# Optimization experiments

Measured on AMD Instinct MI355X. Metric: run time of the kernel, lower is better.

## Reference

```python
import jax, jax.numpy as jnp
import numpy as np

B, T = 32, 64
STOCH, DETER, HIDDEN = 1024, 4096, 1024
ACT_DIM, EMBED = 128, 1536
MIN_STD = 0.1
EPS = 1e-3  # dreamerv3-torch uses LayerNorm(eps=1e-3)


def _ln(x, g, b):
    m = jnp.mean(x, -1, keepdims=True)
    v = jnp.var(x, -1, keepdims=True)
    return (x - m) * jax.lax.rsqrt(v + EPS) * g + b


def setup_inputs() -> dict:
    key = jax.random.key(0)
    ks = jax.random.split(key, 24)

    def w(k, fan_in, fan_out):
        return jax.random.normal(k, (fan_in, fan_out), jnp.float32) / np.sqrt(fan_in)

    inp = {
        "embed": jax.random.normal(ks[0], (B, T, EMBED), jnp.float32),
        "action": jax.random.normal(ks[1], (B, T, ACT_DIM), jnp.float32),
        "is_first": jnp.zeros((B, T), jnp.bool_),
        "init_deter": jax.random.normal(ks[2], (B, DETER), jnp.float32),
        "init_stoch": jax.random.normal(ks[3], (B, STOCH), jnp.float32),
        "noise_prior": jax.random.normal(ks[4], (B, T, STOCH), jnp.float32),
        "noise_post": jax.random.normal(ks[5], (B, T, STOCH), jnp.float32),
        # _img_in_layers: Linear(stoch+act -> hidden, no bias) + LN + SiLU
        "W_in": w(ks[6], STOCH + ACT_DIM, HIDDEN),
        "g_in": 1.0 + 0.1 * jax.random.normal(ks[7], (HIDDEN,), jnp.float32),
        "b_in": 0.1 * jax.random.normal(ks[8], (HIDDEN,), jnp.float32),
        # GRUCell: Linear(hidden+deter -> 3*deter, no bias) + LN
        "W_gru": w(ks[9], HIDDEN + DETER, 3 * DETER),
        "g_gru": 1.0 + 0.1 * jax.random.normal(ks[10], (3 * DETER,), jnp.float32),
        "b_gru": 0.1 * jax.random.normal(ks[11], (3 * DETER,), jnp.float32),
        # _img_out_layers: Linear(deter -> hidden, no bias) + LN + SiLU
        "W_imgout": w(ks[12], DETER, HIDDEN),
        "g_io": 1.0 + 0.1 * jax.random.normal(ks[13], (HIDDEN,), jnp.float32),
        "b_io": 0.1 * jax.random.normal(ks[14], (HIDDEN,), jnp.float32),
        # _obs_out_layers: Linear(deter+embed -> hidden, no bias) + LN + SiLU
        "W_obsout": w(ks[15], DETER + EMBED, HIDDEN),
        "g_oo": 1.0 + 0.1 * jax.random.normal(ks[16], (HIDDEN,), jnp.float32),
        "b_oo": 0.1 * jax.random.normal(ks[17], (HIDDEN,), jnp.float32),
        # suff-stats layers: Linear(hidden -> 2*stoch) with bias
        "W_ims": w(ks[18], HIDDEN, 2 * STOCH),
        "b_ims": 0.01 * jax.random.normal(ks[19], (2 * STOCH,), jnp.float32),
        "W_obs": w(ks[20], HIDDEN, 2 * STOCH),
        "b_obs": 0.01 * jax.random.normal(ks[21], (2 * STOCH,), jnp.float32),
    }
    return inp


def _observe(embed, action, init_deter, init_stoch, noise_prior, noise_post,
             W_in, g_in, b_in, W_gru, g_gru, b_gru, W_imgout, g_io, b_io,
             W_obsout, g_oo, b_oo, W_ims, b_ims, W_obs, b_obs):
    def suff_stats(h, W, b, noise):
        stats = h @ W + b
        mean, std = jnp.split(stats, 2, -1)
        std = jax.nn.softplus(std) + MIN_STD  # std_act='softplus', mean_act='none'
        return mean, std, mean + std * noise

    def step(carry, xs):
        deter, stoch = carry
        e, a, n_p, n_q = xs
        # img_in: concat(prev_stoch, action) -> Linear -> LN -> SiLU
        x = jax.nn.silu(_ln(jnp.concatenate([stoch, a], -1) @ W_in, g_in, b_in))
        # GRUCell with layernorm (update_bias = -1)
        parts = _ln(jnp.concatenate([x, deter], -1) @ W_gru, g_gru, b_gru)
        reset, cand, update = jnp.split(parts, 3, -1)
        reset = jax.nn.sigmoid(reset)
        cand = jnp.tanh(reset * cand)
        update = jax.nn.sigmoid(update - 1.0)
        deter = update * cand + (1.0 - update) * deter
        # prior (imagination) suff stats + sample
        h_p = jax.nn.silu(_ln(deter @ W_imgout, g_io, b_io))
        mean_p, std_p, stoch_p = suff_stats(h_p, W_ims, b_ims, n_p)
        # posterior (observation) suff stats + sample
        h_q = jax.nn.silu(_ln(jnp.concatenate([deter, e], -1) @ W_obsout, g_oo, b_oo))
        mean_q, std_q, stoch_q = suff_stats(h_q, W_obs, b_obs, n_q)
        out = jnp.concatenate([deter, stoch_q, mean_q, std_q, stoch_p, mean_p, std_p], -1)
        return (deter, stoch_q), out

    xs = (jnp.swapaxes(embed, 0, 1), jnp.swapaxes(action, 0, 1),
          jnp.swapaxes(noise_prior, 0, 1), jnp.swapaxes(noise_post, 0, 1))
    _, outs = jax.lax.scan(step, (init_deter, init_stoch), xs)
    return jnp.swapaxes(outs, 0, 1)  # [B, T, deter + 6*stoch]


def reference(embed, action, is_first, init_deter, init_stoch, noise_prior, noise_post,
              W_in, g_in, b_in, W_gru, g_gru, b_gru, W_imgout, g_io, b_io,
              W_obsout, g_oo, b_oo, W_ims, b_ims, W_obs, b_obs):
    # is_first is all-False and state is given, so the init-mixing branch is never taken
    del is_first
    return _observe(embed, action, init_deter, init_stoch, noise_prior, noise_post,
                    W_in, g_in, b_in, W_gru, g_gru, b_gru, W_imgout, g_io, b_io,
                    W_obsout, g_oo, b_oo, W_ims, b_ims, W_obs, b_obs)
```

## Files before the change

### kernel.cpp

```cpp
#include <hip/hip_runtime.h>
#include <hip/hip_bf16.h>

#define T_ 64
#define DETER_ 4096
#define GRUN 12288

typedef __attribute__((ext_vector_type(8))) __bf16 bf16x8;
typedef __attribute__((ext_vector_type(4))) float f32x4;
typedef __attribute__((ext_vector_type(8))) unsigned short u16x8;
typedef __attribute__((ext_vector_type(4))) unsigned short u16x4;

__device__ inline unsigned short f2bf(float f) {
    union { float f; unsigned u; } x; x.f = f;
    unsigned r = x.u + 0x7fffu + ((x.u >> 16) & 1u);
    return (unsigned short)(r >> 16);
}
__device__ inline float sigmoidf_(float v) { return 1.f / (1.f + __expf(-v)); }
__device__ inline float siluf_(float v)    { return v / (1.f + __expf(-v)); }
__device__ inline float softplusf_(float v){ return fmaxf(v, 0.f) + __logf(1.f + __expf(-fabsf(v))); }
__device__ inline float tanhf_(float v)    { return 2.f / (1.f + __expf(-2.f * v)) - 1.f; }

__device__ inline void barrier_() {
    asm volatile("" ::: "memory");
    __builtin_amdgcn_s_barrier();
    asm volatile("" ::: "memory");
}
template <int N> __device__ inline void vmwaitN() {
    asm volatile("s_waitcnt vmcnt(%0)" :: "i"(N) : "memory");
}
__device__ inline void lgkmwait_() {
    asm volatile("s_waitcnt lgkmcnt(0)" ::: "memory");
}


__global__ __launch_bounds__(256) void k_pack(const float* __restrict__ W,
                                              unsigned short* __restrict__ dst,
                                              int K, int N) {
    long fid = (long)blockIdx.x * 256 + threadIdx.x;
    long nfr = (long)K * N / 8;
    if (fid >= nfr) return;
    int lane = (int)(fid & 63);
    long tile = fid >> 6;
    int ktiles = K >> 5;
    int k_t = (int)(tile % ktiles);
    int n_t = (int)(tile / ktiles);
    int c = lane & 15, kb = lane >> 4;
    int k0 = k_t * 32 + kb * 8;
    int n = n_t * 16 + c;
    unsigned short v[8];
#pragma unroll
    for (int i = 0; i < 8; i++) v[i] = f2bf(W[(long)(k0 + i) * N + n]);
    *reinterpret_cast<u16x8*>(dst + fid * 8) = *reinterpret_cast<u16x8*>(v);
}

__global__ __launch_bounds__(256) void k_conv(const float* __restrict__ s,
                                              unsigned short* __restrict__ d, long n) {
    long i = ((long)blockIdx.x * 256 + threadIdx.x) * 4;
    if (i >= n) return;
    f32x4 v = *reinterpret_cast<const f32x4*>(s + i);
    unsigned short o[4];
#pragma unroll
    for (int k = 0; k < 4; k++) o[k] = f2bf(v[k]);
    *reinterpret_cast<u16x4*>(d + i) = *reinterpret_cast<u16x4*>(o);
}

__global__ __launch_bounds__(256) void k_copy(const float* __restrict__ s,
                                              float* __restrict__ d, long n) {
    long i = ((long)blockIdx.x * 256 + threadIdx.x) * 4;
    if (i >= n) return;
    *reinterpret_cast<f32x4*>(d + i) = *reinterpret_cast<const f32x4*>(s + i);
}


template <int CW>
__device__ inline void stage_glds(unsigned short* chunk, const unsigned short* __restrict__ src,
                                  long ld, long k0) {
    constexpr int NI = (32 * CW * 2) / 4096;
    int wv = (int)threadIdx.x >> 6, lane = (int)threadIdx.x & 63;
#pragma unroll
    for (int i = 0; i < NI; ++i) {
        int obase = (wv * NI + i) << 10;
        int o = obase + lane * 16;
        int row = o / (CW * 2);
        int cb = o - row * (CW * 2);
        int gb = cb ^ ((row & 7) << 4);
        const char* ga = (const char*)(src + (long)row * ld + k0) + gb;
        __builtin_amdgcn_global_load_lds(
            (const __attribute__((address_space(1))) void*)ga,
            (__attribute__((address_space(3))) void*)(chunk + (obase >> 1)),
            16, 0, 0);
    }
}

__device__ inline void stage_ln512(unsigned short* chunk, const float* __restrict__ raw,
                                   int ld, int col0,
                                   const float* __restrict__ g, const float* __restrict__ b,
                                   const float* s_mean, const float* s_rstd) {
    int tid = threadIdx.x;
#pragma unroll
    for (int i = 0; i < 8; ++i) {
        int e = tid * 8 + i * 2048;
        int row = e >> 9, col = e & 511;
        float m = s_mean[row], rs = s_rstd[row];
// ... 121 lines not shown
                                       g_ln, b_ln, s_mean, s_rstd);
        if (ch < NG) { if (nx < NG) vmwaitN<NI>(); else vmwaitN<0>(); }
        if (nx >= NG && nx < NCH) lgkmwait_();
        barrier_();
        int kt0 = (ch < NG) ? (ktg0 + ch * (CW / 32)) : ((ch - NG) * 16);
        mfma_rh<CW>(sb[ch & 1], mrow, kb, bbase + (long)kt0 * 512, acc);
        barrier_();
    }
    __syncthreads();
#pragma unroll
    for (int j = 0; j < 4; ++j) s_out[rh * 16 + kb * 4 + j][nt * 16 + c] = acc[j];
    __syncthreads();
    int orow = tid >> 3, c4 = (tid & 7) * 4;
    long rg = rowbase + orow;
    float v[4]; float s = 0.f, q = 0.f;
#pragma unroll
    for (int i = 0; i < 4; ++i) {
        float x = s_out[orow][c4 + i];
        if (addin) x += addin[rg * addin_ld + blockIdx.x * 32 + c4 + i];
        v[i] = x; s += x; q += x * x;
    }
#pragma unroll
    for (int i = 0; i < 4; ++i) outp[rg * out_ld + blockIdx.x * 32 + c4 + i] = v[i];
    if (partials) {
#pragma unroll
        for (int m = 1; m < 8; m <<= 1) { s += __shfl_xor(s, m); q += __shfl_xor(q, m); }
        if ((tid & 7) == 0) {
            partials[((long)blockIdx.x * prows + rg) * 2] = s;
            partials[((long)blockIdx.x * prows + rg) * 2 + 1] = q;
        }
    }
}

__global__ __launch_bounds__(256) void k_gru2(
    const unsigned short* __restrict__ Bp,
    const unsigned short* __restrict__ deterb,
    const float* __restrict__ x_raw, const float* __restrict__ px,
    const float* __restrict__ g_in, const float* __restrict__ b_in,
    float* __restrict__ Gp0, float* __restrict__ Gp1)
{
    __shared__ __align__(16) unsigned short sb[2][32 * 512];
    __shared__ float s_out[32][66];
    __shared__ float s_mean[32], s_rstd[32];
    int tid = threadIdx.x, lane = tid & 63, wv = tid >> 6;
    int c = lane & 15, kb = lane >> 4;
    long ntg = (long)blockIdx.x * 4 + wv;
    const unsigned short* bbase = Bp + ntg * 160 * 512 + lane * 8;
    f32x4 acc0 = {0,0,0,0}, acc1 = {0,0,0,0};

    if (blockIdx.y == 0) {
        if (tid < 32) {
            float s = 0.f, q = 0.f;
            for (int j = 0; j < 32; ++j) {
                s += px[((long)j * 32 + tid) * 2];
                q += px[((long)j * 32 + tid) * 2 + 1];
            }
            float m = s * (1.f / 1024.f);
            s_mean[tid] = m;
            s_rstd[tid] = rsqrtf(q * (1.f / 1024.f) - m * m + 1e-3f);
        }
        __syncthreads();
        stage_glds<512>(sb[0], deterb, 4096, 0);
        stage_glds<512>(sb[1], deterb, 4096, 512);
        vmwaitN<8>(); barrier_();
        mfma2<512>(sb[0], c, kb, bbase + 32 * 512, acc0, acc1);
        barrier_();
        stage_glds<512>(sb[0], deterb, 4096, 1024);
        vmwaitN<8>(); barrier_();
        mfma2<512>(sb[1], c, kb, bbase + 48 * 512, acc0, acc1);
        barrier_();
        stage_ln512(sb[1], x_raw, 1024, 0, g_in, b_in, s_mean, s_rstd);
        vmwaitN<0>(); barrier_();
        mfma2<512>(sb[0], c, kb, bbase + 64 * 512, acc0, acc1);
        barrier_();
        stage_ln512(sb[0], x_raw, 1024, 512, g_in, b_in, s_mean, s_rstd);
        lgkmwait_(); barrier_();
        mfma2<512>(sb[1], c, kb, bbase + 0, acc0, acc1);
        barrier_();
        mfma2<512>(sb[0], c, kb, bbase + 16 * 512, acc0, acc1);
    } else {
        stage_glds<512>(sb[0], deterb, 4096, 1536);
        stage_glds<512>(sb[1], deterb, 4096, 2048);
        vmwaitN<8>(); barrier_();
        mfma2<512>(sb[0], c, kb, bbase + 80 * 512, acc0, acc1);
        barrier_();
        stage_glds<512>(sb[0], deterb, 4096, 2560);
        vmwaitN<8>(); barrier_();
        mfma2<512>(sb[1], c, kb, bbase + 96 * 512, acc0, acc1);
        barrier_();
        stage_glds<512>(sb[1], deterb, 4096, 3072);
        vmwaitN<8>(); barrier_();
        mfma2<512>(sb[0], c, kb, bbase + 112 * 512, acc0, acc1);
        barrier_();
        stage_glds<512>(sb[0], deterb, 4096, 3584);
        vmwaitN<8>(); barrier_();
        mfma2<512>(sb[1], c, kb, bbase + 128 * 512, acc0, acc1);
        barrier_();
        vmwaitN<0>(); barrier_();
        mfma2<512>(sb[0], c, kb, bbase + 144 * 512, acc0, acc1);
    }
    __syncthreads();
#pragma unroll
    for (int j = 0; j < 4; ++j) {
        s_out[kb * 4 + j][wv * 16 + c] = acc0[j];
        s_out[16 + kb * 4 + j][wv * 16 + c] = acc1[j];
    }
    __syncthreads();
    float* G = (blockIdx.y == 0) ? Gp0 : Gp1;
    int row = tid >> 3, c8 = (tid & 7) * 8;
#pragma unroll
    for (int i = 0; i < 8; ++i)
        G[(long)row * GRUN + blockIdx.x * 64 + c8 + i] = s_out[row][c8 + i];
}

__global__ __launch_bounds__(1024) void k_deter2(
    const float* __restrict__ Gp0, const float* __restrict__ Gp1,
    const float* __restrict__ g_gru, const float* __restrict__ b_gru,
    float* __restrict__ deterf, unsigned short* __restrict__ deterb,
    unsigned short* __restrict__ deter_allb, float* __restrict__ out, int t)
{
    __shared__ float gsh[GRUN];
    __shared__ float red[32];
    int r = blockIdx.x, tid = threadIdx.x;
    int lane = tid & 63, wv = tid >> 6;
    const float* a0 = Gp0 + (long)r * GRUN;
    const float* a1 = Gp1 + (long)r * GRUN;
    float s = 0.f, q = 0.f;
#pragma unroll
    for (int i = 0; i < 3; ++i) {
        int col = (tid + i * 1024) * 4;
        f32x4 v = *reinterpret_cast<const f32x4*>(a0 + col);
        v += *reinterpret_cast<const f32x4*>(a1 + col);
        *reinterpret_cast<f32x4*>(gsh + col) = v;
#pragma unroll
        for (int j = 0; j < 4; ++j) { s += v[j]; q += v[j] * v[j]; }
    }
#pragma unroll
    for (int m = 1; m < 64; m <<= 1) { s += __shfl_xor(s, m); q += __shfl_xor(q, m); }
    if (lane == 0) { red[wv] = s; red[16 + wv] = q; }
    __syncthreads();
    float fs = 0.f, fq = 0.f;
#pragma unroll
    for (int i = 0; i < 16; ++i) { fs += red[i]; fq += red[16 + i]; }
    float mean = fs * (1.f / 12288.f);
    float rstd = rsqrtf(fq * (1.f / 12288.f) - mean * mean + 1e-3f);
    long orow = (long)r * T_ + t;
#pragma unroll
    for (int it = 0; it < 2; ++it) {
        int j = tid * 2 + it * 2048;
        float2 rr = *reinterpret_cast<const float2*>(gsh + j);
        float2 cc = *reinterpret_cast<const float2*>(gsh + 4096 + j);
        float2 uu = *reinterpret_cast<const float2*>(gsh + 8192 + j);
        float2 dd = *reinterpret_cast<const float2*>(deterf + (long)r * DETER_ + j);
        float dn[2]; unsigned short db[2];
#pragma unroll
        for (int i = 0; i < 2; ++i) {
            float gv = (i == 0) ? rr.x : rr.y;
            float cv = (i == 0) ? cc.x : cc.y;
            float uv = (i == 0) ? uu.x : uu.y;
            float dv = (i == 0) ? dd.x : dd.y;
            float lr = (gv - mean) * rstd * g_gru[j + i] + b_gru[j + i];
            float lc = (cv - mean) * rstd * g_gru[4096 + j + i] + b_gru[4096 + j + i];
            float lu = (uv - mean) * rstd * g_gru[8192 + j + i] + b_gru[8192 + j + i];
            float reset = sigmoidf_(lr);
            float cand = tanhf_(reset * lc);
            float upd = sigmoidf_(lu - 1.f);
            dn[i] = upd * cand + (1.f - upd) * dv;
            db[i] = f2bf(dn[i]);
        }
        float2 nd; nd.x = dn[0]; nd.y = dn[1];
        *reinterpret_cast<float2*>(deterf + (long)r * DETER_ + j) = nd;
        unsigned pk = (unsigned)db[0] | ((unsigned)db[1] << 16);
        *reinterpret_cast<unsigned*>(deterb + (long)r * DETER_ + j) = pk;
        *reinterpret_cast<unsigned*>(deter_allb + orow * DETER_ + j) = pk;
        *reinterpret_cast<float2*>(out + orow * 10240 + j) = nd;
    }
}

__global__ __launch_bounds__(256) void k_h4(
    const unsigned short* __restrict__ Wood,
    const unsigned short* __restrict__ deterb,
    float* __restrict__ hpart)
{
    __shared__ __align__(16) unsigned short sb[2][32 * 512];
    __shared__ float s_out[32][66];
    int tid = threadIdx.x, lane = tid & 63, wv = tid >> 6;
    int c = lane & 15, kb = lane >> 4;
    int n = blockIdx.x, kq = blockIdx.y;
    const unsigned short* bbase = Wood + ((long)(n * 4 + wv) * 128) * 512 + lane * 8;
    f32x4 acc0 = {0,0,0,0}, acc1 = {0,0,0,0};
    stage_glds<512>(sb[0], deterb, 4096, (long)kq * 1024);
    stage_glds<512>(sb[1], deterb, 4096, (long)kq * 1024 + 512);
    vmwaitN<8>(); barrier_();
    mfma2<512>(sb[0], c, kb, bbase + (long)(kq * 32) * 512, acc0, acc1);
    vmwaitN<0>(); barrier_();
    mfma2<512>(sb[1], c, kb, bbase + (long)(kq * 32 + 16) * 512, acc0, acc1);
    __syncthreads();
#pragma unroll
    for (int j = 0; j < 4; ++j) {
        s_out[kb * 4 + j][wv * 16 + c] = acc0[j];
        s_out[16 + kb * 4 + j][wv * 16 + c] = acc1[j];
    }
    __syncthreads();
    int row = tid >> 3, c8 = (tid & 7) * 8;
    float* hp = hpart + (long)kq * 32768 + (long)row * 1024 + n * 64 + c8;
#pragma unroll
    for (int i = 0; i < 8; ++i) hp[i] = s_out[row][c8 + i];
}

__global__ __launch_bounds__(256) void k_statsq2(
    const unsigned short* __restrict__ Bp, const float* __restrict__ hpart,
    const float* __restrict__ E_pre,
    const float* __restrict__ g_oo, const float* __restrict__ b_oo,
    const float* __restrict__ bias,
    const float* __restrict__ noise, float* __restrict__ out,
    unsigned short* __restrict__ stochb, int t)
{
    __shared__ __align__(16) unsigned short sb[2][32 * 512];
    __shared__ float s_out[32][66];
    __shared__ float s_mean[32], s_rstd[32];
    int tid = threadIdx.x, lane = tid & 63, wv = tid >> 6;
    int c = lane & 15, kb = lane >> 4;
    {
        int row = tid >> 3, c0 = (tid & 7) * 128;
        const float* h0 = hpart + (long)row * 1024 + c0;
        const float* ep = E_pre + ((long)row * T_ + t) * 1024 + c0;
        float s = 0.f, q = 0.f;
#pragma unroll 8
        for (int kk = 0; kk < 128; kk += 4) {
            f32x4 v = *reinterpret_cast<const f32x4*>(h0 + kk);
            v += *reinterpret_cast<const f32x4*>(h0 + 32768 + kk);
            v += *reinterpret_cast<const f32x4*>(h0 + 65536 + kk);
            v += *reinterpret_cast<const f32x4*>(h0 + 98304 + kk);
            v += *reinterpret_cast<const f32x4*>(ep + kk);
#pragma unroll
            for (int j2 = 0; j2 < 4; ++j2) { s += v[j2]; q += v[j2] * v[j2]; }
        }
#pragma unroll
        for (int m = 1; m < 8; m <<= 1) { s += __shfl_xor(s, m); q += __shfl_xor(q, m); }
        if ((tid & 7) == 0) {
            float mm = s * (1.f / 1024.f);
            s_mean[row] = mm;
            s_rstd[row] = rsqrtf(q * (1.f / 1024.f) - mm * mm + 1e-3f);
        }
    }
    __syncthreads();
    int part = wv >> 1, nt = wv & 1;
    long ntg = (long)part * 64 + blockIdx.x * 2 + nt;
    const unsigned short* bbase = Bp + ntg * 32 * 512 + lane * 8;
    f32x4 acc0 = {0,0,0,0}, acc1 = {0,0,0,0};
    stage_lnsum(sb[0], hpart, E_pre, t, 0, g_oo, b_oo, s_mean, s_rstd);
    stage_lnsum(sb[1], hpart, E_pre, t, 512, g_oo, b_oo, s_mean, s_rstd);
    lgkmwait_(); barrier_();
    mfma2<512>(sb[0], c, kb, bbase, acc0, acc1);
    mfma2<512>(sb[1], c, kb, bbase + 16 * 512, acc0, acc1);
    __syncthreads();
    float bv = bias[ntg * 16 + c];
#pragma unroll
    for (int j = 0; j < 4; ++j) {
        s_out[kb * 4 + j][part * 32 + nt * 16 + c] = acc0[j] + bv;
        s_out[16 + kb * 4 + j][part * 32 + nt * 16 + c] = acc1[j] + bv;
    }
    __syncthreads();
    int r = tid >> 3, j0 = (tid & 7) * 4;
    long orow = (long)r * T_ + t;
#pragma unroll
    for (int i = 0; i < 4; ++i) {
        int j = j0 + i;
        float mean = s_out[r][j];
        float sd = softplusf_(s_out[r][32 + j]) + 0.1f;
        int cg2 = blockIdx.x * 32 + j;
        float st = mean + sd * noise[orow * 1024 + cg2];
        float* op = out + orow * 10240;
        op[4096 + cg2] = st; op[5120 + cg2] = mean; op[6144 + cg2] = sd;
        stochb[(long)r * 1024 + cg2] = f2bf(st);
    }
}

__global__ __launch_bounds__(256) void k_bstats(
    const unsigned short* __restrict__ Bp, const unsigned short* __restrict__ h_pb,
    const float* __restrict__ bias, const float* __restrict__ noise,
    float* __restrict__ out)
{
    __shared__ __align__(16) unsigned short sb[2][32 * 512];
    __shared__ float s_out[32][66];
    int tid = threadIdx.x;
    int lane = tid & 63, wv = tid >> 6;
    int part = wv >> 1, nt = wv & 1;
    int c = lane & 15, kb = lane >> 4;
    int s_ = blockIdx.x, rowbase = blockIdx.y * 32;
    const unsigned short* A = h_pb + (long)rowbase * 1024;
    long ntg = (long)part * 64 + s_ * 2 + nt;
    const unsigned short* bbase = Bp + ntg * 32 * 512 + lane * 8;
    f32x4 acc0 = {0.f,0.f,0.f,0.f}, acc1 = {0.f,0.f,0.f,0.f};
    stage_glds<512>(sb[0], A, 1024, 0);
    stage_glds<512>(sb[1], A, 1024, 512);
    vmwaitN<8>(); barrier_();
    mfma_rh<512>(sb[0], c, kb, bbase, acc0);
    mfma_rh<512>(sb[0], 16 + c, kb, bbase, acc1);
    vmwaitN<0>(); barrier_();
    mfma_rh<512>(sb[1], c, kb, bbase + 16 * 512, acc0);
    mfma_rh<512>(sb[1], 16 + c, kb, bbase + 16 * 512, acc1);
    __syncthreads();
    float bv = bias[ntg * 16 + c];
#pragma unroll
    for (int j = 0; j < 4; ++j) {
        s_out[kb * 4 + j][part * 32 + nt * 16 + c] = acc0[j] + bv;
        s_out[16 + kb * 4 + j][part * 32 + nt * 16 + c] = acc1[j] + bv;
// ... 69 lines not shown
    float* out = (float*)d_out;

    char* ws = (char*)d_ws;
    size_t off = 0;
    auto alloc = [&](size_t bytes) {
        size_t r = off;
        off = (off + bytes + 255) & ~(size_t)255;
        return r;
    };
    unsigned short* pWgru  = (unsigned short*)(ws + alloc((size_t)5120 * 12288 * 2));
    unsigned short* pWin_s = (unsigned short*)(ws + alloc((size_t)1024 * 1024 * 2));
    unsigned short* pWin_a = (unsigned short*)(ws + alloc((size_t)128 * 1024 * 2));
    unsigned short* pWio   = (unsigned short*)(ws + alloc((size_t)4096 * 1024 * 2));
    unsigned short* pWood  = (unsigned short*)(ws + alloc((size_t)4096 * 1024 * 2));
    unsigned short* pWooe  = (unsigned short*)(ws + alloc((size_t)1536 * 1024 * 2));
    unsigned short* pWims  = (unsigned short*)(ws + alloc((size_t)1024 * 2048 * 2));
    unsigned short* pWobs  = (unsigned short*)(ws + alloc((size_t)1024 * 2048 * 2));
    unsigned short* act_bf = (unsigned short*)(ws + alloc((size_t)2048 * 128 * 2));
    unsigned short* emb_bf = (unsigned short*)(ws + alloc((size_t)2048 * 1536 * 2));
    float* A_pre  = (float*)(ws + alloc((size_t)2048 * 1024 * 4));
    float* E_pre  = (float*)(ws + alloc((size_t)2048 * 1024 * 4));
    float* x_raw  = (float*)(ws + alloc((size_t)32 * 1024 * 4));
    float* Gp0    = (float*)(ws + alloc((size_t)32 * GRUN * 4));
    float* Gp1    = (float*)(ws + alloc((size_t)32 * GRUN * 4));
    float* deterf = (float*)(ws + alloc((size_t)32 * DETER_ * 4));
    unsigned short* deterb     = (unsigned short*)(ws + alloc((size_t)32 * DETER_ * 2));
    unsigned short* deter_allb = (unsigned short*)(ws + alloc((size_t)2048 * DETER_ * 2));
    unsigned short* stochb = (unsigned short*)(ws + alloc((size_t)32 * 1024 * 2));
    float* hp_raw = (float*)(ws + alloc((size_t)2048 * 1024 * 4));
    unsigned short* h_pb = (unsigned short*)(ws + alloc((size_t)2048 * 1024 * 2));
    float* px  = (float*)(ws + alloc((size_t)32 * 32 * 2 * 4));
    float* pbh = (float*)(ws + alloc((size_t)32 * 2048 * 2 * 4));
    float* hpart = (float*)(ws + alloc((size_t)4 * 32 * 1024 * 4));
    (void)ws_size; (void)out_size; (void)n_in; (void)in_sizes;

    auto packgrid = [](long K, long N) { return (unsigned)((K * N / 8 + 255) / 256); };

    k_pack<<<packgrid(5120, 12288), 256, 0, stream>>>(W_gru, pWgru, 5120, 12288);
    k_pack<<<packgrid(1024, 1024), 256, 0, stream>>>(W_in, pWin_s, 1024, 1024);
    k_pack<<<packgrid(128, 1024), 256, 0, stream>>>(W_in + (size_t)1024 * 1024, pWin_a, 128, 1024);
    k_pack<<<packgrid(4096, 1024), 256, 0, stream>>>(W_io, pWio, 4096, 1024);
    k_pack<<<packgrid(4096, 1024), 256, 0, stream>>>(W_oo, pWood, 4096, 1024);
    k_pack<<<packgrid(1536, 1024), 256, 0, stream>>>(W_oo + (size_t)4096 * 1024, pWooe, 1536, 1024);
    k_pack<<<packgrid(1024, 2048), 256, 0, stream>>>(W_ims, pWims, 1024, 2048);
    k_pack<<<packgrid(1024, 2048), 256, 0, stream>>>(W_obs, pWobs, 1024, 2048);
    k_conv<<<(2048 * 128 / 4 + 255) / 256, 256, 0, stream>>>(action, act_bf, 2048L * 128);
    k_conv<<<(2048 * 1536 / 4 + 255) / 256, 256, 0, stream>>>(embed, emb_bf, 2048L * 1536);
    k_conv<<<(32 * 1024 / 4 + 255) / 256, 256, 0, stream>>>(init_stoch, stochb, 32L * 1024);
    k_conv<<<(32 * 4096 / 4 + 255) / 256, 256, 0, stream>>>(init_deter, deterb, 32L * 4096);
    k_copy<<<(32 * 4096 / 4 + 255) / 256, 256, 0, stream>>>(init_deter, deterf, 32L * 4096);
    k_gemm32<128, 1, 0><<<dim3(32, 64), 256, 0, stream>>>(
        pWin_a, 4, 0, act_bf, 128, nullptr, 0, nullptr, nullptr, nullptr, 0,
        nullptr, 0, A_pre, 1024, nullptr, 0);
    k_gemm32<512, 3, 0><<<dim3(32, 64), 256, 0, stream>>>(
        pWooe, 48, 0, emb_bf, 1536, nullptr, 0, nullptr, nullptr, nullptr, 0,
        nullptr, 0, E_pre, 1024, nullptr, 0);

    for (int t = 0; t < T_; ++t) {
        k_gemm32<512, 2, 0><<<dim3(32, 1), 256, 0, stream>>>(
            pWin_s, 32, 0, stochb, 1024, nullptr, 0, nullptr, nullptr, nullptr, 0,
            A_pre + (size_t)t * 1024, (long)T_ * 1024, x_raw, 1024, px, 32);
        k_gru2<<<dim3(192, 2), 256, 0, stream>>>(pWgru, deterb, x_raw, px, g_in, b_in,
                                                 Gp0, Gp1);
        k_deter2<<<32, 1024, 0, stream>>>(Gp0, Gp1, g_gru, b_gru, deterf, deterb,
                                          deter_allb, out, t);
        k_h4<<<dim3(16, 4), 256, 0, stream>>>(pWood, deterb, hpart);
        k_statsq2<<<32, 256, 0, stream>>>(pWobs, hpart, E_pre, g_oo, b_oo, b_obs,
                                          noise_po, out, stochb, t);
    }

    k_gemm32<512, 8, 0><<<dim3(32, 64), 256, 0, stream>>>(
        pWio, 128, 0, deter_allb, 4096, nullptr, 0, nullptr, nullptr, nullptr, 0,
        nullptr, 0, hp_raw, 1024, pbh, 2048);
    k_bfin<<<256, 256, 0, stream>>>(hp_raw, pbh, g_io, b_io, h_pb);
    k_bstats<<<dim3(32, 64), 256, 0, stream>>>(pWims, h_pb, b_ims, noise_pr, out);
}
```

Before: 7.000 ms.

## Fuse per-step recurrent kernels into two launches with intra-kernel flag synchronization

Cuts the per-timestep work from five kernel launches to two. The input projection GEMM is merged into the GRU kernel. The deter update, the obs-out GEMM and the posterior stats are merged into one kernel, with global atomic flags used for inter-block dependencies in place of kernel boundaries. GRU blocks also do their deter-only partial product before waiting on the x flag, so that work overlaps the x computation. This removes launch overhead and inter-kernel gaps per step. The risk is deadlock if dependent blocks are not co-resident, plus some spin-wait cost.

```diff
diff --git a/kernel.cpp b/kernel.cpp
--- a/kernel.cpp
+++ b/kernel.cpp
@@ -30,6 +30,19 @@
 }
 __device__ inline void lgkmwait_() {
     asm volatile("s_waitcnt lgkmcnt(0)" ::: "memory");
+}
+
+__device__ inline void waitflag(int* f, int target) {
+    if (threadIdx.x == 0) {
+        while (__hip_atomic_load(f, __ATOMIC_ACQUIRE, __HIP_MEMORY_SCOPE_AGENT) < target)
+            __builtin_amdgcn_s_sleep(2);
+    }
+    __syncthreads();
+}
+__device__ inline void postflag(int* f) {
+    __syncthreads();
+    if (threadIdx.x == 0)
+        __hip_atomic_fetch_add(f, 1, __ATOMIC_RELEASE, __HIP_MEMORY_SCOPE_AGENT);
 }
 
 
@@ -69,6 +82,11 @@
     long i = ((long)blockIdx.x * 256 + threadIdx.x) * 4;
     if (i >= n) return;
     *reinterpret_cast<f32x4*>(d + i) = *reinterpret_cast<const f32x4*>(s + i);
+}
+
+__global__ void k_zeroflags(int* f, int n) {
+    int i = blockIdx.x * 256 + threadIdx.x;
+    if (i < n) f[i] = 0;
 }
 
 
@@ -256,26 +274,76 @@
     }
 }
 
-__global__ __launch_bounds__(256) void k_gru2(
-    const unsigned short* __restrict__ Bp,
+__global__ __launch_bounds__(256) void k_gruxf(
+    const unsigned short* __restrict__ pWin_s,
+    const unsigned short* __restrict__ pWgru,
+    const unsigned short* __restrict__ stochb,
     const unsigned short* __restrict__ deterb,
-    const float* __restrict__ x_raw, const float* __restrict__ px,
+    const float* __restrict__ A_pre,
+    float* __restrict__ x_raw, float* __restrict__ px,
     const float* __restrict__ g_in, const float* __restrict__ b_in,
-    float* __restrict__ Gp0, float* __restrict__ Gp1)
+    float* __restrict__ Gp0, float* __restrict__ Gp1,
+    int* __restrict__ fX, int t)
 {
     __shared__ __align__(16) unsigned short sb[2][32 * 512];
     __shared__ float s_out[32][66];
     __shared__ float s_mean[32], s_rstd[32];
-    int tid = threadIdx.x, lane = tid & 63, wv = tid >> 6;
+    int bid = blockIdx.x, tid = threadIdx.x;
+    int lane = tid & 63, wv = tid >> 6;
     int c = lane & 15, kb = lane >> 4;
-    long ntg = (long)blockIdx.x * 4 + wv;
-    const unsigned short* bbase = Bp + ntg * 160 * 512 + lane * 8;
-    f32x4 acc0 = {0,0,0,0}, acc1 = {0,0,0,0};
-
-    if (blockIdx.y == 0) {
+
+    if (bid < 16) {
+        int xi = bid;
+        const unsigned short* bbase = pWin_s + ((long)xi * 4 + wv) * 32 * 512 + lane * 8;
+        f32x4 a0 = {0, 0, 0, 0}, a1 = {0, 0, 0, 0};
+        stage_glds<512>(sb[0], stochb, 1024, 0);
+        stage_glds<512>(sb[1], stochb, 1024, 512);
+        vmwaitN<8>(); barrier_();
+        mfma2<512>(sb[0], c, kb, bbase, a0, a1);
+        vmwaitN<0>(); barrier_();
+        mfma2<512>(sb[1], c, kb, bbase + (long)16 * 512, a0, a1);
+        __syncthreads();
+#pragma unroll
+        for (int j = 0; j < 4; ++j) {
+            s_out[kb * 4 + j][wv * 16 + c] = a0[j];
+            s_out[16 + kb * 4 + j][wv * 16 + c] = a1[j];
+        }
+        __syncthreads();
+        int row = tid >> 3, c8 = (tid & 7) * 8;
+        const float* ap = A_pre + ((long)row * T_ + t) * 1024 + xi * 64 + c8;
+        float s = 0.f, q = 0.f, v[8];
+#pragma unroll
+        for (int i = 0; i < 8; ++i) {
+            float x = s_out[row][c8 + i] + ap[i];
+            v[i] = x; s += x; q += x * x;
+        }
+#pragma unroll
+        for (int i = 0; i < 8; ++i) x_raw[(long)row * 1024 + xi * 64 + c8 + i] = v[i];
+#pragma unroll
+        for (int m = 1; m < 8; m <<= 1) { s += __shfl_xor(s, m); q += __shfl_xor(q, m); }
+        if ((tid & 7) == 0) {
+            px[((long)xi * 32 + row) * 2] = s;
+            px[((long)xi * 32 + row) * 2 + 1] = q;
+        }
+        postflag(&fX[t]);
+    } else if (bid < 208) {
+        int gb = bid - 16;
+        long ntg = (long)gb * 4 + wv;
+        const unsigned short* bbase = pWgru + ntg * 160 * 512 + lane * 8;
+        f32x4 acc0 = {0, 0, 0, 0}, acc1 = {0, 0, 0, 0};
+        stage_glds<512>(sb[0], deterb, 4096, 0);
+        stage_glds<512>(sb[1], deterb, 4096, 512);
+        vmwaitN<8>(); barrier_();
+        mfma2<512>(sb[0], c, kb, bbase + 32 * 512, acc0, acc1);
+        barrier_();
+        stage_glds<512>(sb[0], deterb, 4096, 1024);
+        vmwaitN<8>(); barrier_();
+        mfma2<512>(sb[1], c, kb, bbase + 48 * 512, acc0, acc1);
+        barrier_();
+        waitflag(&fX[t], 16);
         if (tid < 32) {
             float s = 0.f, q = 0.f;
-            for (int j = 0; j < 32; ++j) {
+            for (int j = 0; j < 16; ++j) {
                 s += px[((long)j * 32 + tid) * 2];
                 q += px[((long)j * 32 + tid) * 2 + 1];
             }
@@ -284,15 +352,6 @@
             s_rstd[tid] = rsqrtf(q * (1.f / 1024.f) - m * m + 1e-3f);
         }
         __syncthreads();
-        stage_glds<512>(sb[0], deterb, 4096, 0);
-        stage_glds<512>(sb[1], deterb, 4096, 512);
-        vmwaitN<8>(); barrier_();
-        mfma2<512>(sb[0], c, kb, bbase + 32 * 512, acc0, acc1);
-        barrier_();
-        stage_glds<512>(sb[0], deterb, 4096, 1024);
-        vmwaitN<8>(); barrier_();
-        mfma2<512>(sb[1], c, kb, bbase + 48 * 512, acc0, acc1);
-        barrier_();
         stage_ln512(sb[1], x_raw, 1024, 0, g_in, b_in, s_mean, s_rstd);
         vmwaitN<0>(); barrier_();
         mfma2<512>(sb[0], c, kb, bbase + 64 * 512, acc0, acc1);
@@ -302,7 +361,22 @@
         mfma2<512>(sb[1], c, kb, bbase + 0, acc0, acc1);
         barrier_();
         mfma2<512>(sb[0], c, kb, bbase + 16 * 512, acc0, acc1);
+        __syncthreads();
+#pragma unroll
+        for (int j = 0; j < 4; ++j) {
+            s_out[kb * 4 + j][wv * 16 + c] = acc0[j];
+            s_out[16 + kb * 4 + j][wv * 16 + c] = acc1[j];
+        }
+        __syncthreads();
+        int row = tid >> 3, c8 = (tid & 7) * 8;
+#pragma unroll
+        for (int i = 0; i < 8; ++i)
+            Gp0[(long)row * GRUN + gb * 64 + c8 + i] = s_out[row][c8 + i];
     } else {
+        int gb = bid - 208;
+        long ntg = (long)gb * 4 + wv;
+        const unsigned short* bbase = pWgru + ntg * 160 * 512 + lane * 8;
+        f32x4 acc0 = {0, 0, 0, 0}, acc1 = {0, 0, 0, 0};
         stage_glds<512>(sb[0], deterb, 4096, 1536);
         stage_glds<512>(sb[1], deterb, 4096, 2048);
         vmwaitN<8>(); barrier_();
@@ -322,182 +396,173 @@
         barrier_();
         vmwaitN<0>(); barrier_();
         mfma2<512>(sb[0], c, kb, bbase + 144 * 512, acc0, acc1);
-    }
-    __syncthreads();
-#pragma unroll
-    for (int j = 0; j < 4; ++j) {
-        s_out[kb * 4 + j][wv * 16 + c] = acc0[j];
-        s_out[16 + kb * 4 + j][wv * 16 + c] = acc1[j];
-    }
-    __syncthreads();
-    float* G = (blockIdx.y == 0) ? Gp0 : Gp1;
-    int row = tid >> 3, c8 = (tid & 7) * 8;
-#pragma unroll
-    for (int i = 0; i < 8; ++i)
-        G[(long)row * GRUN + blockIdx.x * 64 + c8 + i] = s_out[row][c8 + i];
-}
-
-__global__ __launch_bounds__(1024) void k_deter2(
+        __syncthreads();
+#pragma unroll
+        for (int j = 0; j < 4; ++j) {
+            s_out[kb * 4 + j][wv * 16 + c] = acc0[j];
+            s_out[16 + kb * 4 + j][wv * 16 + c] = acc1[j];
+        }
+        __syncthreads();
+        int row = tid >> 3, c8 = (tid & 7) * 8;
+#pragma unroll
+        for (int i = 0; i < 8; ++i)
+            Gp1[(long)row * GRUN + gb * 64 + c8 + i] = s_out[row][c8 + i];
+    }
+}
+
+__global__ __launch_bounds__(256) void k_dhs(
     const float* __restrict__ Gp0, const float* __restrict__ Gp1,
     const float* __restrict__ g_gru, const float* __restrict__ b_gru,
     float* __restrict__ deterf, unsigned short* __restrict__ deterb,
-    unsigned short* __restrict__ deter_allb, float* __restrict__ out, int t)
+    unsigned short* __restrict__ deter_allb,
+    const unsigned short* __restrict__ pWood, float* __restrict__ hpart,
+    const unsigned short* __restrict__ pWobs, const float* __restrict__ E_pre,
+    const float* __restrict__ g_oo, const float* __restrict__ b_oo,
+    const float* __restrict__ b_obs, const float* __restrict__ noise_po,
+    float* __restrict__ out, unsigned short* __restrict__ stochb,
+    int* __restrict__ fD, int* __restrict__ fH, int t)
 {
-    __shared__ float gsh[GRUN];
-    __shared__ float red[32];
-    int r = blockIdx.x, tid = threadIdx.x;
+    __shared__ __align__(16) char smem[74240];
+    unsigned short (*sb)[32 * 512] = reinterpret_cast<unsigned short(*)[32 * 512]>(smem);
+    float (*s_out)[66] = reinterpret_cast<float(*)[66]>(smem + 65536);
+    float* s_mean = reinterpret_cast<float*>(smem + 65536 + 8448);
+    float* s_rstd = s_mean + 32;
+    float* gsh = reinterpret_cast<float*>(smem);
+    float* red = reinterpret_cast<float*>(smem + 49152);
+
+    int bid = blockIdx.x, tid = threadIdx.x;
     int lane = tid & 63, wv = tid >> 6;
-    const float* a0 = Gp0 + (long)r * GRUN;
-    const float* a1 = Gp1 + (long)r * GRUN;
-    float s = 0.f, q = 0.f;
-#pragma unroll
-    for (int i = 0; i < 3; ++i) {
-        int col = (tid + i * 1024) * 4;
-        f32x4 v = *reinterpret_cast<const f32x4*>(a0 + col);
-        v += *reinterpret_cast<const f32x4*>(a1 + col);
-        *reinterpret_cast<f32x4*>(gsh + col) = v;
-#pragma unroll
-        for (int j = 0; j < 4; ++j) { s += v[j]; q += v[j] * v[j]; }
-    }
-#pragma unroll
-    for (int m = 1; m < 64; m <<= 1) { s += __shfl_xor(s, m); q += __shfl_xor(q, m); }
-    if (lane == 0) { red[wv] = s; red[16 + wv] = q; }
-    __syncthreads();
-    float fs = 0.f, fq = 0.f;
-#pragma unroll
-    for (int i = 0; i < 16; ++i) { fs += red[i]; fq += red[16 + i]; }
-    float mean = fs * (1.f / 12288.f);
-    float rstd = rsqrtf(fq * (1.f / 12288.f) - mean * mean + 1e-3f);
-    long orow = (long)r * T_ + t;
-#pragma unroll
-    for (int it = 0; it < 2; ++it) {
-        int j = tid * 2 + it * 2048;
-        float2 rr = *reinterpret_cast<const float2*>(gsh + j);
-        float2 cc = *reinterpret_cast<const float2*>(gsh + 4096 + j);
-        float2 uu = *reinterpret_cast<const float2*>(gsh + 8192 + j);
-        float2 dd = *reinterpret_cast<const float2*>(deterf + (long)r * DETER_ + j);
-        float dn[2]; unsigned short db[2];
-#pragma unroll
-        for (int i = 0; i < 2; ++i) {
-            float gv = (i == 0) ? rr.x : rr.y;
-            float cv = (i == 0) ? cc.x : cc.y;
-            float uv = (i == 0) ? uu.x : uu.y;
-            float dv = (i == 0) ? dd.x : dd.y;
-            float lr = (gv - mean) * rstd * g_gru[j + i] + b_gru[j + i];
-            float lc = (cv - mean) * rstd * g_gru[4096 + j + i] + b_gru[4096 + j + i];
-            float lu = (uv - mean) * rstd * g_gru[8192 + j + i] + b_gru[8192 + j + i];
-            float reset = sigmoidf_(lr);
-            float cand = tanhf_(reset * lc);
-            float upd = sigmoidf_(lu - 1.f);
-            dn[i] = upd * cand + (1.f - upd) * dv;
-            db[i] = f2bf(dn[i]);
-        }
-        float2 nd; nd.x = dn[0]; nd.y = dn[1];
-        *reinterpret_cast<float2*>(deterf + (long)r * DETER_ + j) = nd;
-        unsigned pk = (unsigned)db[0] | ((unsigned)db[1] << 16);
-        *reinterpret_cast<unsigned*>(deterb + (long)r * DETER_ + j) = pk;
-        *reinterpret_cast<unsigned*>(deter_allb + orow * DETER_ + j) = pk;
-        *reinterpret_cast<float2*>(out + orow * 10240 + j) = nd;
-    }
-}
-
-__global__ __launch_bounds__(256) void k_h4(
-    const unsigned short* __restrict__ Wood,
-    const unsigned short* __restrict__ deterb,
-    float* __restrict__ hpart)
-{
-    __shared__ __align__(16) unsigned short sb[2][32 * 512];
-    __shared__ float s_out[32][66];
-    int tid = threadIdx.x, lane = tid & 63, wv = tid >> 6;
     int c = lane & 15, kb = lane >> 4;
-    int n = blockIdx.x, kq = blockIdx.y;
-    const unsigned short* bbase = Wood + ((long)(n * 4 + wv) * 128) * 512 + lane * 8;
-    f32x4 acc0 = {0,0,0,0}, acc1 = {0,0,0,0};
-    stage_glds<512>(sb[0], deterb, 4096, (long)kq * 1024);
-    stage_glds<512>(sb[1], deterb, 4096, (long)kq * 1024 + 512);
-    vmwaitN<8>(); barrier_();
-    mfma2<512>(sb[0], c, kb, bbase + (long)(kq * 32) * 512, acc0, acc1);
-    vmwaitN<0>(); barrier_();
-    mfma2<512>(sb[1], c, kb, bbase + (long)(kq * 32 + 16) * 512, acc0, acc1);
-    __syncthreads();
-#pragma unroll
-    for (int j = 0; j < 4; ++j) {
-        s_out[kb * 4 + j][wv * 16 + c] = acc0[j];
-        s_out[16 + kb * 4 + j][wv * 16 + c] = acc1[j];
-    }
-    __syncthreads();
-    int row = tid >> 3, c8 = (tid & 7) * 8;
-    float* hp = hpart + (long)kq * 32768 + (long)row * 1024 + n * 64 + c8;
-#pragma unroll
-    for (int i = 0; i < 8; ++i) hp[i] = s_out[row][c8 + i];
-}
-
-__global__ __launch_bounds__(256) void k_statsq2(
-    const unsigned short* __restrict__ Bp, const float* __restrict__ hpart,
-    const float* __restrict__ E_pre,
-    const float* __restrict__ g_oo, const float* __restrict__ b_oo,
-    const float* __restrict__ bias,
-    const float* __restrict__ noise, float* __restrict__ out,
-    unsigned short* __restrict__ stochb, int t)
-{
-    __shared__ __align__(16) unsigned short sb[2][32 * 512];
-    __shared__ float s_out[32][66];
-    __shared__ float s_mean[32], s_rstd[32];
-    int tid = threadIdx.x, lane = tid & 63, wv = tid >> 6;
-    int c = lane & 15, kb = lane >> 4;
-    {
-        int row = tid >> 3, c0 = (tid & 7) * 128;
-        const float* h0 = hpart + (long)row * 1024 + c0;
-        const float* ep = E_pre + ((long)row * T_ + t) * 1024 + c0;
+
+    if (bid < 32) {
+        int r = bid;
+        const float* g0 = Gp0 + (long)r * GRUN;
+        const float* g1 = Gp1 + (long)r * GRUN;
         float s = 0.f, q = 0.f;
+#pragma unroll
+        for (int i = 0; i < 12; ++i) {
+            int col = tid * 4 + i * 1024;
+            f32x4 v = *reinterpret_cast<const f32x4*>(g0 + col);
+            v += *reinterpret_cast<const f32x4*>(g1 + col);
+            *reinterpret_cast<f32x4*>(gsh + col) = v;
+#pragma unroll
+            for (int j = 0; j < 4; ++j) { s += v[j]; q += v[j] * v[j]; }
+        }
+#pragma unroll
+        for (int m = 1; m < 64; m <<= 1) { s += __shfl_xor(s, m); q += __shfl_xor(q, m); }
+        if (lane == 0) { red[wv] = s; red[4 + wv] = q; }
+        __syncthreads();
+        float fs = red[0] + red[1] + red[2] + red[3];
+        float fq = red[4] + red[5] + red[6] + red[7];
+        float mean = fs * (1.f / 12288.f);
+        float rstd = rsqrtf(fq * (1.f / 12288.f) - mean * mean + 1e-3f);
+        long orow = (long)r * T_ + t;
+#pragma unroll
+        for (int it = 0; it < 4; ++it) {
+            int j = tid * 4 + it * 1024;
+            f32x4 rr = *reinterpret_cast<const f32x4*>(gsh + j);
+            f32x4 cc = *reinterpret_cast<const f32x4*>(gsh + 4096 + j);
+            f32x4 uu = *reinterpret_cast<const f32x4*>(gsh + 8192 + j);
+            f32x4 dd = *reinterpret_cast<const f32x4*>(deterf + (long)r * DETER_ + j);
+            f32x4 nd; unsigned short db[4];
+#pragma unroll
+            for (int i = 0; i < 4; ++i) {
+                float lr = (rr[i] - mean) * rstd * g_gru[j + i] + b_gru[j + i];
+                float lc = (cc[i] - mean) * rstd * g_gru[4096 + j + i] + b_gru[4096 + j + i];
+                float lu = (uu[i] - mean) * rstd * g_gru[8192 + j + i] + b_gru[8192 + j + i];
+                float reset = sigmoidf_(lr);
+                float cand = tanhf_(reset * lc);
+                float upd = sigmoidf_(lu - 1.f);
+                nd[i] = upd * cand + (1.f - upd) * dd[i];
+                db[i] = f2bf(nd[i]);
+            }
+            *reinterpret_cast<f32x4*>(deterf + (long)r * DETER_ + j) = nd;
+            *reinterpret_cast<u16x4*>(deterb + (long)r * DETER_ + j) = *reinterpret_cast<u16x4*>(db);
+            *reinterpret_cast<u16x4*>(deter_allb + orow * DETER_ + j) = *reinterpret_cast<u16x4*>(db);
+            *reinterpret_cast<f32x4*>(out + orow * 10240 + j) = nd;
+        }
+        postflag(&fD[t]);
+    } else if (bid < 96) {
+        int idx = bid - 32;
+        int n = idx & 15, kq = idx >> 4;
+        const unsigned short* bbase = pWood + ((long)(n * 4 + wv) * 128) * 512 + lane * 8;
+        waitflag(&fD[t], 32);
+        f32x4 acc0 = {0, 0, 0, 0}, acc1 = {0, 0, 0, 0};
+        stage_glds<512>(sb[0], deterb, 4096, (long)kq * 1024);
+        stage_glds<512>(sb[1], deterb, 4096, (long)kq * 1024 + 512);
+        vmwaitN<8>(); barrier_();
+        mfma2<512>(sb[0], c, kb, bbase + (long)(kq * 32) * 512, acc0, acc1);
+        vmwaitN<0>(); barrier_();
+        mfma2<512>(sb[1], c, kb, bbase + (long)(kq * 32 + 16) * 512, acc0, acc1);
+        __syncthreads();
+#pragma unroll
+        for (int j = 0; j < 4; ++j) {
+            s_out[kb * 4 + j][wv * 16 + c] = acc0[j];
+            s_out[16 + kb * 4 + j][wv * 16 + c] = acc1[j];
+        }
+        __syncthreads();
+        int row = tid >> 3, c8 = (tid & 7) * 8;
+        float* hp = hpart + (long)kq * 32768 + (long)row * 1024 + n * 64 + c8;
+#pragma unroll
+        for (int i = 0; i < 8; ++i) hp[i] = s_out[row][c8 + i];
+        postflag(&fH[t]);
+    } else {
+        int s_ = bid - 96;
+        waitflag(&fH[t], 64);
+        {
+            int row = tid >> 3, c0 = (tid & 7) * 128;
+            const float* h0 = hpart + (long)row * 1024 + c0;
+            const float* ep = E_pre + ((long)row * T_ + t) * 1024 + c0;
+            float s = 0.f, q = 0.f;
 #pragma unroll 8
-        for (int kk = 0; kk < 128; kk += 4) {
-            f32x4 v = *reinterpret_cast<const f32x4*>(h0 + kk);
-            v += *reinterpret_cast<const f32x4*>(h0 + 32768 + kk);
-            v += *reinterpret_cast<const f32x4*>(h0 + 65536 + kk);
-            v += *reinterpret_cast<const f32x4*>(h0 + 98304 + kk);
-            v += *reinterpret_cast<const f32x4*>(ep + kk);
-#pragma unroll
-            for (int j2 = 0; j2 < 4; ++j2) { s += v[j2]; q += v[j2] * v[j2]; }
-        }
-#pragma unroll
-        for (int m = 1; m < 8; m <<= 1) { s += __shfl_xor(s, m); q += __shfl_xor(q, m); }
-        if ((tid & 7) == 0) {
-            float mm = s * (1.f / 1024.f);
-            s_mean[row] = mm;
-            s_rstd[row] = rsqrtf(q * (1.f / 1024.f) - mm * mm + 1e-3f);
-        }
-    }
-    __syncthreads();
-    int part = wv >> 1, nt = wv & 1;
-    long ntg = (long)part * 64 + blockIdx.x * 2 + nt;
-    const unsigned short* bbase = Bp + ntg * 32 * 512 + lane * 8;
-    f32x4 acc0 = {0,0,0,0}, acc1 = {0,0,0,0};
-    stage_lnsum(sb[0], hpart, E_pre, t, 0, g_oo, b_oo, s_mean, s_rstd);
-    stage_lnsum(sb[1], hpart, E_pre, t, 512, g_oo, b_oo, s_mean, s_rstd);
-    lgkmwait_(); barrier_();
-    mfma2<512>(sb[0], c, kb, bbase, acc0, acc1);
-    mfma2<512>(sb[1], c, kb, bbase + 16 * 512, acc0, acc1);
-    __syncthreads();
-    float bv = bias[ntg * 16 + c];
-#pragma unroll
-    for (int j = 0; j < 4; ++j) {
-        s_out[kb * 4 + j][part * 32 + nt * 16 + c] = acc0[j] + bv;
-        s_out[16 + kb * 4 + j][part * 32 + nt * 16 + c] = acc1[j] + bv;
-    }
-    __syncthreads();
-    int r = tid >> 3, j0 = (tid & 7) * 4;
-    long orow = (long)r * T_ + t;
-#pragma unroll
-    for (int i = 0; i < 4; ++i) {
-        int j = j0 + i;
-        float mean = s_out[r][j];
-        float sd = softplusf_(s_out[r][32 + j]) + 0.1f;
-        int cg2 = blockIdx.x * 32 + j;
-        float st = mean + sd * noise[orow * 1024 + cg2];
-        float* op = out + orow * 10240;
-        op[4096 + cg2] = st; op[5120 + cg2] = mean; op[6144 + cg2] = sd;
-        stochb[(long)r * 1024 + cg2] = f2bf(st);
+            for (int kk = 0; kk < 128; kk += 4) {
+                f32x4 v = *reinterpret_cast<const f32x4*>(h0 + kk);
+                v += *reinterpret_cast<const f32x4*>(h0 + 32768 + kk);
+                v += *reinterpret_cast<const f32x4*>(h0 + 65536 + kk);
+                v += *reinterpret_cast<const f32x4*>(h0 + 98304 + kk);
+                v += *reinterpret_cast<const f32x4*>(ep + kk);
+#pragma unroll
+                for (int j2 = 0; j2 < 4; ++j2) { s += v[j2]; q += v[j2] * v[j2]; }
+            }
+#pragma unroll
+            for (int m = 1; m < 8; m <<= 1) { s += __shfl_xor(s, m); q += __shfl_xor(q, m); }
+            if ((tid & 7) == 0) {
+                float mm = s * (1.f / 1024.f);
+                s_mean[row] = mm;
+                s_rstd[row] = rsqrtf(q * (1.f / 1024.f) - mm * mm + 1e-3f);
+            }
+        }
+        __syncthreads();
+        int part = wv >> 1, nt = wv & 1;
+        long ntg = (long)part * 64 + s_ * 2 + nt;
+        const unsigned short* bbase = pWobs + ntg * 32 * 512 + lane * 8;
+        f32x4 acc0 = {0, 0, 0, 0}, acc1 = {0, 0, 0, 0};
+        stage_lnsum(sb[0], hpart, E_pre, t, 0, g_oo, b_oo, s_mean, s_rstd);
+        stage_lnsum(sb[1], hpart, E_pre, t, 512, g_oo, b_oo, s_mean, s_rstd);
+        lgkmwait_(); barrier_();
+        mfma2<512>(sb[0], c, kb, bbase, acc0, acc1);
+        mfma2<512>(sb[1], c, kb, bbase + 16 * 512, acc0, acc1);
+        __syncthreads();
+        float bv = b_obs[ntg * 16 + c];
+#pragma unroll
+        for (int j = 0; j < 4; ++j) {
+            s_out[kb * 4 + j][part * 32 + nt * 16 + c] = acc0[j] + bv;
+            s_out[16 + kb * 4 + j][part * 32 + nt * 16 + c] = acc1[j] + bv;
+        }
+        __syncthreads();
+        int r = tid >> 3, j0 = (tid & 7) * 4;
+        long orow = (long)r * T_ + t;
+#pragma unroll
+        for (int i = 0; i < 4; ++i) {
+            int j = j0 + i;
+            float mean = s_out[r][j];
+            float sd = softplusf_(s_out[r][32 + j]) + 0.1f;
+            int cg2 = s_ * 32 + j;
+            float st = mean + sd * noise_po[orow * 1024 + cg2];
+            float* op = out + orow * 10240;
+            op[4096 + cg2] = st; op[5120 + cg2] = mean; op[6144 + cg2] = sd;
+            stochb[(long)r * 1024 + cg2] = f2bf(st);
+        }
     }
 }
 
@@ -633,6 +698,8 @@
     float* px  = (float*)(ws + alloc((size_t)32 * 32 * 2 * 4));
     float* pbh = (float*)(ws + alloc((size_t)32 * 2048 * 2 * 4));
     float* hpart = (float*)(ws + alloc((size_t)4 * 32 * 1024 * 4));
+    int* flags = (int*)(ws + alloc((size_t)3 * 64 * 4));
+    int* fX = flags, *fD = flags + 64, *fH = flags + 128;
     (void)ws_size; (void)out_size; (void)n_in; (void)in_sizes;
 
     auto packgrid = [](long K, long N) { return (unsigned)((K * N / 8 + 255) / 256); };
@@ -656,18 +723,15 @@
     k_gemm32<512, 3, 0><<<dim3(32, 64), 256, 0, stream>>>(
         pWooe, 48, 0, emb_bf, 1536, nullptr, 0, nullptr, nullptr, nullptr, 0,
         nullptr, 0, E_pre, 1024, nullptr, 0);
+    k_zeroflags<<<1, 256, 0, stream>>>(flags, 3 * 64);
 
     for (int t = 0; t < T_; ++t) {
-        k_gemm32<512, 2, 0><<<dim3(32, 1), 256, 0, stream>>>(
-            pWin_s, 32, 0, stochb, 1024, nullptr, 0, nullptr, nullptr, nullptr, 0,
-            A_pre + (size_t)t * 1024, (long)T_ * 1024, x_raw, 1024, px, 32);
-        k_gru2<<<dim3(192, 2), 256, 0, stream>>>(pWgru, deterb, x_raw, px, g_in, b_in,
-                                                 Gp0, Gp1);
-        k_deter2<<<32, 1024, 0, stream>>>(Gp0, Gp1, g_gru, b_gru, deterf, deterb,
-                                          deter_allb, out, t);
-        k_h4<<<dim3(16, 4), 256, 0, stream>>>(pWood, deterb, hpart);
-        k_statsq2<<<32, 256, 0, stream>>>(pWobs, hpart, E_pre, g_oo, b_oo, b_obs,
-                                          noise_po, out, stochb, t);
+        k_gruxf<<<400, 256, 0, stream>>>(pWin_s, pWgru, stochb, deterb, A_pre,
+                                         x_raw, px, g_in, b_in, Gp0, Gp1, fX, t);
+        k_dhs<<<128, 256, 0, stream>>>(Gp0, Gp1, g_gru, b_gru, deterf, deterb,
+                                       deter_allb, pWood, hpart, pWobs, E_pre,
+                                       g_oo, b_oo, b_obs, noise_po, out, stochb,
+                                       fD, fH, t);
     }
 
     k_gemm32<512, 8, 0><<<dim3(32, 64), 256, 0, stream>>>(
```

Result: slower. 8.247 ms (+17.8%).

## Single-buffer LDS staging and alias output tile to raise occupancy

Applied to the files above, without the earlier changes.

Three GEMV-style kernels drop their double-buffered 64KB shared staging to one 32KB buffer. The epilogue output tile now reuses that same buffer, and launch bounds request 4 blocks per CU. The aim is to fit more resident blocks per CU so memory latency is hidden by occupancy rather than intra-block prefetch. In exchange, each chunk now waits fully for its load before compute, which serializes staging and MFMA within a block.

```diff
diff --git a/kernel.cpp b/kernel.cpp
--- a/kernel.cpp
+++ b/kernel.cpp
@@ -256,15 +256,16 @@
     }
 }
 
-__global__ __launch_bounds__(256) void k_gru2(
+__global__ __launch_bounds__(256, 4) void k_gru2(
     const unsigned short* __restrict__ Bp,
     const unsigned short* __restrict__ deterb,
     const float* __restrict__ x_raw, const float* __restrict__ px,
     const float* __restrict__ g_in, const float* __restrict__ b_in,
     float* __restrict__ Gp0, float* __restrict__ Gp1)
 {
-    __shared__ __align__(16) unsigned short sb[2][32 * 512];
-    __shared__ float s_out[32][66];
+    __shared__ __align__(16) char smem[32768];
+    unsigned short* sbuf = reinterpret_cast<unsigned short*>(smem);
+    float (*s_out)[66] = reinterpret_cast<float(*)[66]>(smem);
     __shared__ float s_mean[32], s_rstd[32];
     int tid = threadIdx.x, lane = tid & 63, wv = tid >> 6;
     int c = lane & 15, kb = lane >> 4;
@@ -284,44 +285,28 @@
             s_rstd[tid] = rsqrtf(q * (1.f / 1024.f) - m * m + 1e-3f);
         }
         __syncthreads();
-        stage_glds<512>(sb[0], deterb, 4096, 0);
-        stage_glds<512>(sb[1], deterb, 4096, 512);
-        vmwaitN<8>(); barrier_();
-        mfma2<512>(sb[0], c, kb, bbase + 32 * 512, acc0, acc1);
+#pragma unroll
+        for (int ch = 0; ch < 3; ++ch) {
+            stage_glds<512>(sbuf, deterb, 4096, (long)ch * 512);
+            vmwaitN<0>(); barrier_();
+            mfma2<512>(sbuf, c, kb, bbase + (long)(32 + ch * 16) * 512, acc0, acc1);
+            barrier_();
+        }
+        stage_ln512(sbuf, x_raw, 1024, 0, g_in, b_in, s_mean, s_rstd);
+        lgkmwait_(); barrier_();
+        mfma2<512>(sbuf, c, kb, bbase, acc0, acc1);
         barrier_();
-        stage_glds<512>(sb[0], deterb, 4096, 1024);
-        vmwaitN<8>(); barrier_();
-        mfma2<512>(sb[1], c, kb, bbase + 48 * 512, acc0, acc1);
-        barrier_();
-        stage_ln512(sb[1], x_raw, 1024, 0, g_in, b_in, s_mean, s_rstd);
-        vmwaitN<0>(); barrier_();
-        mfma2<512>(sb[0], c, kb, bbase + 64 * 512, acc0, acc1);
-        barrier_();
-        stage_ln512(sb[0], x_raw, 1024, 512, g_in, b_in, s_mean, s_rstd);
+        stage_ln512(sbuf, x_raw, 1024, 512, g_in, b_in, s_mean, s_rstd);
         lgkmwait_(); barrier_();
-        mfma2<512>(sb[1], c, kb, bbase + 0, acc0, acc1);
-        barrier_();
-        mfma2<512>(sb[0], c, kb, bbase + 16 * 512, acc0, acc1);
+        mfma2<512>(sbuf, c, kb, bbase + (long)16 * 512, acc0, acc1);
     } else {
-        stage_glds<512>(sb[0], deterb, 4096, 1536);
-        stage_glds<512>(sb[1], deterb, 4096, 2048);
-        vmwaitN<8>(); barrier_();
-        mfma2<512>(sb[0], c, kb, bbase + 80 * 512, acc0, acc1);
-        barrier_();
-        stage_glds<512>(sb[0], deterb, 4096, 2560);
-        vmwaitN<8>(); barrier_();
-        mfma2<512>(sb[1], c, kb, bbase + 96 * 512, acc0, acc1);
-        barrier_();
-        stage_glds<512>(sb[1], deterb, 4096, 3072);
-        vmwaitN<8>(); barrier_();
-        mfma2<512>(sb[0], c, kb, bbase + 112 * 512, acc0, acc1);
-        barrier_();
-        stage_glds<512>(sb[0], deterb, 4096, 3584);
-        vmwaitN<8>(); barrier_();
-        mfma2<512>(sb[1], c, kb, bbase + 128 * 512, acc0, acc1);
-        barrier_();
-        vmwaitN<0>(); barrier_();
-        mfma2<512>(sb[0], c, kb, bbase + 144 * 512, acc0, acc1);
+#pragma unroll
+        for (int ch = 0; ch < 5; ++ch) {
+            stage_glds<512>(sbuf, deterb, 4096, 1536 + (long)ch * 512);
+            vmwaitN<0>(); barrier_();
+            mfma2<512>(sbuf, c, kb, bbase + (long)(80 + ch * 16) * 512, acc0, acc1);
+            barrier_();
+        }
     }
     __syncthreads();
 #pragma unroll
@@ -401,24 +386,26 @@
     }
 }
 
-__global__ __launch_bounds__(256) void k_h4(
+__global__ __launch_bounds__(256, 4) void k_h4(
     const unsigned short* __restrict__ Wood,
     const unsigned short* __restrict__ deterb,
     float* __restrict__ hpart)
 {
-    __shared__ __align__(16) unsigned short sb[2][32 * 512];
-    __shared__ float s_out[32][66];
+    __shared__ __align__(16) char smem[32768];
+    unsigned short* sbuf = reinterpret_cast<unsigned short*>(smem);
+    float (*s_out)[66] = reinterpret_cast<float(*)[66]>(smem);
     int tid = threadIdx.x, lane = tid & 63, wv = tid >> 6;
     int c = lane & 15, kb = lane >> 4;
     int n = blockIdx.x, kq = blockIdx.y;
     const unsigned short* bbase = Wood + ((long)(n * 4 + wv) * 128) * 512 + lane * 8;
     f32x4 acc0 = {0,0,0,0}, acc1 = {0,0,0,0};
-    stage_glds<512>(sb[0], deterb, 4096, (long)kq * 1024);
-    stage_glds<512>(sb[1], deterb, 4096, (long)kq * 1024 + 512);
-    vmwaitN<8>(); barrier_();
-    mfma2<512>(sb[0], c, kb, bbase + (long)(kq * 32) * 512, acc0, acc1);
+    stage_glds<512>(sbuf, deterb, 4096, (long)kq * 1024);
     vmwaitN<0>(); barrier_();
-    mfma2<512>(sb[1], c, kb, bbase + (long)(kq * 32 + 16) * 512, acc0, acc1);
+    mfma2<512>(sbuf, c, kb, bbase + (long)(kq * 32) * 512, acc0, acc1);
+    barrier_();
+    stage_glds<512>(sbuf, deterb, 4096, (long)kq * 1024 + 512);
+    vmwaitN<0>(); barrier_();
+    mfma2<512>(sbuf, c, kb, bbase + (long)(kq * 32 + 16) * 512, acc0, acc1);
     __syncthreads();
 #pragma unroll
     for (int j = 0; j < 4; ++j) {
@@ -432,7 +419,7 @@
     for (int i = 0; i < 8; ++i) hp[i] = s_out[row][c8 + i];
 }
 
-__global__ __launch_bounds__(256) void k_statsq2(
+__global__ __launch_bounds__(256, 4) void k_statsq2(
     const unsigned short* __restrict__ Bp, const float* __restrict__ hpart,
     const float* __restrict__ E_pre,
     const float* __restrict__ g_oo, const float* __restrict__ b_oo,
@@ -440,8 +427,9 @@
     const float* __restrict__ noise, float* __restrict__ out,
     unsigned short* __restrict__ stochb, int t)
 {
-    __shared__ __align__(16) unsigned short sb[2][32 * 512];
-    __shared__ float s_out[32][66];
+    __shared__ __align__(16) char smem[32768];
+    unsigned short* sbuf = reinterpret_cast<unsigned short*>(smem);
+    float (*s_out)[66] = reinterpret_cast<float(*)[66]>(smem);
     __shared__ float s_mean[32], s_rstd[32];
     int tid = threadIdx.x, lane = tid & 63, wv = tid >> 6;
     int c = lane & 15, kb = lane >> 4;
@@ -473,11 +461,13 @@
     long ntg = (long)part * 64 + blockIdx.x * 2 + nt;
     const unsigned short* bbase = Bp + ntg * 32 * 512 + lane * 8;
     f32x4 acc0 = {0,0,0,0}, acc1 = {0,0,0,0};
-    stage_lnsum(sb[0], hpart, E_pre, t, 0, g_oo, b_oo, s_mean, s_rstd);
-    stage_lnsum(sb[1], hpart, E_pre, t, 512, g_oo, b_oo, s_mean, s_rstd);
+    stage_lnsum(sbuf, hpart, E_pre, t, 0, g_oo, b_oo, s_mean, s_rstd);
     lgkmwait_(); barrier_();
-    mfma2<512>(sb[0], c, kb, bbase, acc0, acc1);
-    mfma2<512>(sb[1], c, kb, bbase + 16 * 512, acc0, acc1);
+    mfma2<512>(sbuf, c, kb, bbase, acc0, acc1);
+    barrier_();
+    stage_lnsum(sbuf, hpart, E_pre, t, 512, g_oo, b_oo, s_mean, s_rstd);
+    lgkmwait_(); barrier_();
+    mfma2<512>(sbuf, c, kb, bbase + 16 * 512, acc0, acc1);
     __syncthreads();
     float bv = bias[ntg * 16 + c];
 #pragma unroll
```

New measurement: 7.423 ms. 1.06x slower.
